# Kernel optimization log

Measured on AMD Instinct MI355X. Metric: run time of the kernel, lower is better.

## Reference

```python
import jax, jax.numpy as jnp
import numpy as np

UNITS = 1024
VOCAB = 50000
EMB = 512
SEQ = 256
BATCH = 256


def setup_inputs() -> dict:
    key = jax.random.key(0)
    ks = jax.random.split(key, 9)
    s = lambda fan_in: 1.0 / np.sqrt(fan_in)
    return {
        "sentences": jax.random.randint(ks[0], (BATCH, SEQ), 0, VOCAB),
        "emb_table": jax.random.normal(ks[1], (VOCAB, EMB), jnp.float32) * 0.05,
        # gate order: i, f, g(cell candidate), o
        "Wx": jax.random.normal(ks[2], (EMB, 4 * UNITS), jnp.float32) * s(EMB),
        "Wh": jax.random.normal(ks[3], (UNITS, 4 * UNITS), jnp.float32) * s(UNITS),
        "b": jnp.zeros((4 * UNITS,), jnp.float32),
        "W1": jax.random.normal(ks[4], (UNITS, 64), jnp.float32) * s(UNITS),
        "b1": jnp.zeros((64,), jnp.float32),
        "W2": jax.random.normal(ks[5], (64, 1), jnp.float32) * s(64),
        "b2": jnp.zeros((1,), jnp.float32),
    }


def _lstm_forward(emb_x, Wx, Wh, b):
    # emb_x: [B, T, E] -> final hidden state [B, U]
    B = emb_x.shape[0]
    U = Wh.shape[0]
    # precompute input projections for all timesteps: [T, B, 4U]
    x_proj = jnp.einsum('bte,eg->tbg', emb_x, Wx) + b

    def step(carry, xp):
        h, c = carry
        gates = xp + h @ Wh  # [B, 4U]
        i, f, g, o = jnp.split(gates, 4, axis=-1)
        i = jax.nn.sigmoid(i)
        f = jax.nn.sigmoid(f)
        g = jnp.tanh(g)
        o = jax.nn.sigmoid(o)
        c = f * c + i * g
        h = o * jnp.tanh(c)
        return (h, c), None

    h0 = jnp.zeros((B, U), emb_x.dtype)
    c0 = jnp.zeros((B, U), emb_x.dtype)
    (h, _), _ = jax.lax.scan(step, (h0, c0), x_proj)
    return h


def reference(sentences, emb_table, Wx, Wh, b, W1, b1, W2, b2):
    emb_x = emb_table[sentences]           # [B, T, E]
    h = _lstm_forward(emb_x, Wx, Wh, b)    # [B, U]
    hidden = h @ W1 + b1                   # Dense(64), linear activation
    logits = hidden @ W2 + b2              # Dense(1)
    return jax.nn.sigmoid(logits)          # [B, 1]
```

## Files before the change

kernel.cpp:

```cpp
#include <hip/hip_runtime.h>

#define B_ 256
#define T_ 256
#define E_ 512
#define U_ 1024
#define G_ 4096
#define V_ 50000
#define TC_ 32
#define NCH_ 8
#define NG_ 8
#define NS_ 32

typedef __bf16 bf16x8 __attribute__((ext_vector_type(8)));
typedef float f32x4 __attribute__((ext_vector_type(4)));
typedef unsigned short us8 __attribute__((ext_vector_type(8)));

__device__ __forceinline__ unsigned short f2bf(float f) {
  union { float f; unsigned u; } v; v.f = f;
  unsigned u = v.u;
  u = (u + 0x7FFFu + ((u >> 16) & 1u)) >> 16;
  return (unsigned short)u;
}
__device__ __forceinline__ float bf2f(unsigned short h) {
  union { unsigned u; float f; } v; v.u = ((unsigned)h) << 16;
  return v.f;
}
__device__ __forceinline__ float sigm_(float x) { return 1.f / (1.f + __expf(-x)); }
__device__ __forceinline__ float tanh_(float x) { return 2.f / (1.f + __expf(-2.f * x)) - 1.f; }

__device__ __forceinline__ void gload16(const void* g, void* l) {
  __builtin_amdgcn_global_load_lds((const __attribute__((address_space(1))) void*)g,
                                   (__attribute__((address_space(3))) void*)l, 16, 0, 0);
}
__device__ __forceinline__ void gload16c(const void* g, void* l) {
  __builtin_amdgcn_global_load_lds((const __attribute__((address_space(1))) void*)g,
                                   (__attribute__((address_space(3))) void*)l, 16, 0, 1);
}

__device__ __forceinline__ int orig_col3(int p) {
  return (((p >> 5) & 3) << 10) + ((p >> 7) << 5) + (p & 31);
}

__global__ void cvt_bf16_kernel(const float* __restrict__ in, unsigned short* __restrict__ out, long n) {
  long i = (((long)blockIdx.x * blockDim.x) + threadIdx.x) << 3;
  long stride = ((long)gridDim.x * blockDim.x) << 3;
  for (; i < n; i += stride) {
    float4 x = *(const float4*)(in + i);
    float4 y = *(const float4*)(in + i + 4);
    us8 v;
    v[0] = f2bf(x.x); v[1] = f2bf(x.y); v[2] = f2bf(x.z); v[3] = f2bf(x.w);
    v[4] = f2bf(y.x); v[5] = f2bf(y.y); v[6] = f2bf(y.z); v[7] = f2bf(y.w);
    *(us8*)(out + i) = v;
  }
}

__global__ void pack_wx_kernel(const float* __restrict__ w, unsigned short* __restrict__ out, int total) {
  int t = blockIdx.x * blockDim.x + threadIdx.x;
  if (t >= total) return;
  int kb = t >> 12, n = t & 4095;
  int oc = orig_col3(n);
  us8 v;
#pragma unroll
  for (int ki = 0; ki < 8; ki++) v[ki] = f2bf(w[(size_t)(kb * 8 + ki) * G_ + oc]);
  *(us8*)(out + (size_t)t * 8) = v;
}

__global__ void pack_wh4_kernel(const float* __restrict__ w, unsigned short* __restrict__ out) {
  int t = blockIdx.x * blockDim.x + threadIdx.x;
  int lane = t & 63;
  int nt  = (t >> 6) & 3;
  int ks  = (t >> 8) & 7;
  int ksl = (t >> 11) & 3;
  int nh  = (t >> 13) & 1;
  int s   = t >> 14;
  int k0 = ksl * 256 + ks * 32 + (lane >> 4) * 8;
  int oc = orig_col3(s * 128 + nh * 64 + nt * 16 + (lane & 15));
  us8 v;
#pragma unroll
  for (int i = 0; i < 8; i++) v[i] = f2bf(w[(size_t)(k0 + i) * G_ + oc]);
  *(us8*)(out + (size_t)t * 8) = v;
}

#define XP_BM 128
#define XP_BN 128
#define XP_KC 64
__global__ __launch_bounds__(256, 2) void xproj_kernel(
    const int* __restrict__ sent, const unsigned short* __restrict__ embb,
    const unsigned short* __restrict__ wxp, const float* __restrict__ bias,
    unsigned short* __restrict__ xp, int t0)
{
  __shared__ __align__(16) unsigned short sA[2][XP_BM * XP_KC];
  __shared__ __align__(16) unsigned short sB[2][XP_KC * XP_BN];
  __shared__ int tok[XP_BM];

  const int tid = threadIdx.x;
  const int lane = tid & 63;
  const int wid = tid >> 6;
  const int m0 = blockIdx.x * XP_BM;
  const int n0 = blockIdx.y * XP_BN;

  if (tid < XP_BM) {
    int row = m0 + tid;
    int tl = row >> 8, b = row & 255;
    tok[tid] = sent[b * T_ + t0 + tl];
  }
  __syncthreads();

  auto stageA = [&](int bf, int kc) {
#pragma unroll
    for (int ii = 0; ii < 4; ii++) {
      int i = wid * 4 + ii;
      int m = i * 8 + (lane >> 3);
      int cl = lane & 7;
      gload16(embb + (size_t)tok[m] * E_ + kc + ((cl ^ (m & 7)) << 3), &sA[bf][i * 512]);
    }
  };
  auto stageB = [&](int bf, int kc) {
    int kb0 = kc >> 3;
#pragma unroll
    for (int jj = 0; jj < 4; jj++) {
      int j = wid * 4 + jj;
      int r = j >> 1;
      int nl = ((j & 1) << 6) + lane;
      int n = nl ^ r;
      gload16(wxp + ((size_t)(kb0 + r) * G_ + n0 + n) * 8, &sB[bf][j * 512]);
    }
  };

  f32x4 acc[4][4];
#pragma unroll
  for (int i = 0; i < 4; i++)
#pragma unroll
    for (int j = 0; j < 4; j++) acc[i][j] = f32x4{0.f, 0.f, 0.f, 0.f};

  const int wm = wid >> 1, wn = wid & 1;

  stageA(0, 0); stageB(0, 0);
  for (int it = 0; it < E_ / XP_KC; it++) {
    int bf = it & 1;
    __syncthreads();
    if (it < E_ / XP_KC - 1) { stageA(bf ^ 1, (it + 1) * XP_KC); stageB(bf ^ 1, (it + 1) * XP_KC); }
#pragma unroll
    for (int kk = 0; kk < 2; kk++) {
      int c = (kk << 2) + (lane >> 4);
      bf16x8 a[4], b[4];
#pragma unroll
      for (int ms = 0; ms < 4; ms++) {
        int m = (wm << 6) + (ms << 4) + (lane & 15);
        a[ms] = *(const bf16x8*)&sA[bf][m * 64 + ((c ^ (m & 7)) << 3)];
      }
#pragma unroll
      for (int ns = 0; ns < 4; ns++) {
        int n = (wn << 6) + (ns << 4) + (lane & 15);
        b[ns] = *(const bf16x8*)&sB[bf][((c << 7) + (n ^ c)) << 3];
      }
#pragma unroll
      for (int ms = 0; ms < 4; ms++)
#pragma unroll
        for (int ns = 0; ns < 4; ns++)
          acc[ms][ns] = __builtin_amdgcn_mfma_f32_16x16x32_bf16(a[ms], b[ns], acc[ms][ns], 0, 0, 0);
    }
  }

#pragma unroll
  for (int ns = 0; ns < 4; ns++) {
    int col = n0 + (wn << 6) + (ns << 4) + (lane & 15);
    float bv = bias[orig_col3(col)];
#pragma unroll
    for (int ms = 0; ms < 4; ms++) {
      int rbase = m0 + (wm << 6) + (ms << 4) + ((lane >> 4) << 2);
#pragma unroll
      for (int rr = 0; rr < 4; rr++)
        xp[(size_t)(rbase + rr) * G_ + col] = f2bf(acc[ms][ns][rr] + bv);
    }
  }
}

__global__ __launch_bounds__(512, 2) void scan_kernel(
    const unsigned short* __restrict__ xpc,
    const unsigned short* __restrict__ whp4,
    unsigned short* __restrict__ hbuf,
    float* __restrict__ cst,
    int* __restrict__ flags,
    int t0)
{
  __shared__ __align__(16) unsigned short sA[32 * 1024];
  __shared__ float sEx[4][32][131];

  const int tid = threadIdx.x, lane = tid & 63, w = tid >> 6;
  const int ksl = w & 3, nh = w >> 2;
  const int g = (int)blockIdx.x & 7, s = (int)blockIdx.x >> 3;
  const int m0g = g * 32, u0 = s * 32;
  const int rx = lane & 7, hi = lane >> 4, lo = lane & 15;

  bf16x8 wh[8][4];
  {
    const bf16x8* wb = (const bf16x8*)whp4 + ((((size_t)s * 2 + nh) * 4 + ksl) * 32) * 64;
#pragma unroll
    for (int ks = 0; ks < 8; ks++)
#pragma unroll
      for (int nt = 0; nt < 4; nt++)
        wh[ks][nt] = wb[(ks * 4 + nt) * 64 + lane];
  }

  const int r_e = tid >> 4, ue = (tid & 15) * 2;
  const size_t ci = (size_t)(m0g + r_e) * U_ + u0 + ue;
  float c0v = cst[ci], c1v = cst[ci + 1];

  const char* abase0 = (const char*)sA + (size_t)lo * 2048;
  const char* abase1 = abase0 + 16 * 2048;

  for (int ts = 0; ts < TC_; ts++) {
    const int t = t0 + ts;

    const unsigned short* xb = xpc + ((size_t)ts * B_ + (m0g + r_e)) * G_ + s * 128;
    unsigned xiv = *(const unsigned*)(xb + ue);
    unsigned xfv = *(const unsigned*)(xb + 32 + ue);
    unsigned xgv = *(const unsigned*)(xb + 64 + ue);
    unsigned xov = *(const unsigned*)(xb + 96 + ue);

    if (t > 0) {
      const int* fp = flags + g * 32 + (lane & 31);
      int v;
      do { v = __hip_atomic_load(fp, __ATOMIC_RELAXED, __HIP_MEMORY_SCOPE_AGENT); }
      while (__any(v < t));
    }

    const unsigned short* hsrc = hbuf + (size_t)(t & 1) * (B_ * U_) + (size_t)m0g * U_;
#pragma unroll
    for (int jj = 0; jj < 8; jj++) {
      int j = w * 8 + jj;
      int r = j >> 1, k2 = j & 1;
      gload16c(hsrc + (size_t)r * U_ + (((k2 << 6) | (lane ^ (r & 7))) << 3),
               &sA[r * 1024 + k2 * 512]);
    }
    __syncthreads();

    f32x4 acc[2][4];
#pragma unroll
    for (int mt = 0; mt < 2; mt++)
#pragma unroll
      for (int nt = 0; nt < 4; nt++) acc[mt][nt] = f32x4{0.f, 0.f, 0.f, 0.f};
#pragma unroll
    for (int ks = 0; ks < 8; ks++) {
      int c = ksl * 32 + ks * 4 + hi;
      int off = (c ^ rx) << 4;
      bf16x8 a0 = *(const bf16x8*)(abase0 + off);
      bf16x8 a1 = *(const bf16x8*)(abase1 + off);
#pragma unroll
      for (int nt = 0; nt < 4; nt++) {
        acc[0][nt] = __builtin_amdgcn_mfma_f32_16x16x32_bf16(a0, wh[ks][nt], acc[0][nt], 0, 0, 0);
        acc[1][nt] = __builtin_amdgcn_mfma_f32_16x16x32_bf16(a1, wh[ks][nt], acc[1][nt], 0, 0, 0);
      }
    }

#pragma unroll
    for (int mt = 0; mt < 2; mt++)
#pragma unroll
      for (int nt = 0; nt < 4; nt++)
#pragma unroll
        for (int rr = 0; rr < 4; rr++)
          sEx[ksl][mt * 16 + hi * 4 + rr][nh * 64 + nt * 16 + lo] = acc[mt][nt][rr];
    __syncthreads();

    {
      float cn[2]; unsigned hv = 0;
#pragma unroll
      for (int j = 0; j < 2; j++) {
        int u = ue + j;
        float gi = sEx[0][r_e][u]      + sEx[1][r_e][u]      + sEx[2][r_e][u]      + sEx[3][r_e][u]      + bf2f((unsigned short)(j ? (xiv >> 16) : xiv));
        float gf = sEx[0][r_e][32 + u] + sEx[1][r_e][32 + u] + sEx[2][r_e][32 + u] + sEx[3][r_e][32 + u] + bf2f((unsigned short)(j ? (xfv >> 16) : xfv));
        float gg = sEx[0][r_e][64 + u] + sEx[1][r_e][64 + u] + sEx[2][r_e][64 + u] + sEx[3][r_e][64 + u] + bf2f((unsigned short)(j ? (xgv >> 16) : xgv));
        float go = sEx[0][r_e][96 + u] + sEx[1][r_e][96 + u] + sEx[2][r_e][96 + u] + sEx[3][r_e][96 + u] + bf2f((unsigned short)(j ? (xov >> 16) : xov));
        float co = j ? c1v : c0v;
        float cv = sigm_(gf) * co + sigm_(gi) * tanh_(gg);
        cn[j] = cv;
        hv |= (unsigned)f2bf(sigm_(go) * tanh_(cv)) << (16 * j);
      }
      c0v = cn[0]; c1v = cn[1];
      *(unsigned*)(hbuf + (size_t)((t + 1) & 1) * (B_ * U_) + ci) = hv;
    }
    __syncthreads();
    if (tid == 0)
      __hip_atomic_store(flags + g * 32 + s, t + 1, __ATOMIC_RELAXED, __HIP_MEMORY_SCOPE_AGENT);
  }

  cst[ci] = c0v; cst[ci + 1] = c1v;
}

__global__ __launch_bounds__(256) void dense_kernel(
    const unsigned short* __restrict__ h, const float* __restrict__ W1, const float* __restrict__ b1,
    const float* __restrict__ W2, const float* __restrict__ b2, float* __restrict__ out)
{
  int tid = threadIdx.x, j = tid & 63, kq = tid >> 6;
  const unsigned short* hr = h + (size_t)blockIdx.x * U_;
  float s = 0.f;
#pragma unroll 8
  for (int k = kq * 256; k < kq * 256 + 256; k++) s += bf2f(hr[k]) * W1[k * 64 + j];
  __shared__ float red[4][64];
  red[kq][j] = s;
  __syncthreads();
  if (tid < 64) {
    float hid = red[0][j] + red[1][j] + red[2][j] + red[3][j] + b1[j];
    float p = hid * W2[j];
#pragma unroll
    for (int off = 32; off; off >>= 1) p += __shfl_down(p, off, 64);
    if (j == 0) out[blockIdx.x] = 1.f / (1.f + __expf(-(p + b2[0])));
  }
}

extern "C" void kernel_launch(void* const* d_in, const int* in_sizes, int n_in,
                              void* d_out, int out_size, void* d_ws, size_t ws_size,
                              hipStream_t stream) {
  const int*   sent = (const int*)d_in[0];
  const float* emb  = (const float*)d_in[1];
  const float* Wx   = (const float*)d_in[2];
  const float* Wh   = (const float*)d_in[3];
  const float* bias = (const float*)d_in[4];
  const float* W1   = (const float*)d_in[5];
  const float* b1   = (const float*)d_in[6];
  const float* W2   = (const float*)d_in[7];
  const float* b2   = (const float*)d_in[8];
  float* out = (float*)d_out;

  char* ws = (char*)d_ws;
  size_t off = 0;
  auto alloc = [&](size_t bytes) { void* p = ws + off; off += (bytes + 255) & ~(size_t)255; return p; };
  unsigned short* embb = (unsigned short*)alloc((size_t)V_ * E_ * 2);
  unsigned short* wxp  = (unsigned short*)alloc((size_t)E_ * G_ * 2);
  unsigned short* whp4 = (unsigned short*)alloc((size_t)U_ * G_ * 2);
  unsigned short* xpc  = (unsigned short*)alloc((size_t)TC_ * B_ * G_ * 2);
  unsigned short* hbuf = (unsigned short*)alloc((size_t)2 * B_ * U_ * 2);
  float*          cst  = (float*)alloc((size_t)B_ * U_ * 4);
  int*            flg  = (int*)alloc((size_t)NG_ * 32 * 4);

  hipLaunchKernelGGL(cvt_bf16_kernel, dim3(12500), dim3(256), 0, stream, emb, embb, (long)V_ * E_);
  hipLaunchKernelGGL(pack_wx_kernel, dim3((E_ / 8) * G_ / 256), dim3(256), 0, stream, Wx, wxp, (E_ / 8) * G_);
  hipLaunchKernelGGL(pack_wh4_kernel, dim3(2048), dim3(256), 0, stream, Wh, whp4);
  hipMemsetAsync(hbuf, 0, (size_t)B_ * U_ * 2, stream);
  hipMemsetAsync(cst, 0, (size_t)B_ * U_ * 4, stream);
  hipMemsetAsync(flg, 0, (size_t)NG_ * 32 * 4, stream);

  for (int ch = 0; ch < NCH_; ch++) {
    hipLaunchKernelGGL(xproj_kernel, dim3(TC_ * B_ / XP_BM, G_ / XP_BN), dim3(256), 0, stream,
                       sent, embb, wxp, bias, xpc, ch * TC_);
    hipLaunchKernelGGL(scan_kernel, dim3(NG_ * NS_), dim3(512), 0, stream,
                       xpc, whp4, hbuf, cst, flg, ch * TC_);
  }
  hipLaunchKernelGGL(dense_kernel, dim3(B_), dim3(256), 0, stream,
                     hbuf , W1, b1, W2, b2, out);
}
```

Before: 1.561 ms.

## Replace per-block flag polling with per-step atomic counters and per-wave h loads

Each step's inter-block sync now uses a per-(timestep, group) atomic counter. A single lane polls it and releases the other waves through a shared-memory flag, replacing polling of 32 flags by every wave. Each wave now loads only its own K-slice of h into a private LDS region and waits on vmcnt, removing a block-wide __syncthreads before the MFMA loop. The spin loop has an iteration cap, and visibility of h written by other blocks relies on relaxed atomics, so there is some ordering risk.

```diff
diff --git a/kernel.cpp b/kernel.cpp
--- a/kernel.cpp
+++ b/kernel.cpp
@@ -181,17 +181,19 @@
     const unsigned short* __restrict__ whp4,
     unsigned short* __restrict__ hbuf,
     float* __restrict__ cst,
-    int* __restrict__ flags,
+    int* __restrict__ cnt,
     int t0)
 {
-  __shared__ __align__(16) unsigned short sA[32 * 1024];
+  __shared__ __align__(16) unsigned short sA[4][32][256];
   __shared__ float sEx[4][32][131];
+  __shared__ int sready;
 
   const int tid = threadIdx.x, lane = tid & 63, w = tid >> 6;
   const int ksl = w & 3, nh = w >> 2;
   const int g = (int)blockIdx.x & 7, s = (int)blockIdx.x >> 3;
   const int m0g = g * 32, u0 = s * 32;
-  const int rx = lane & 7, hi = lane >> 4, lo = lane & 15;
+  const int hi = lane >> 4, lo = lane & 15;
+  const int rx = lo & 7;
 
   bf16x8 wh[8][4];
   {
@@ -207,8 +209,11 @@
   const size_t ci = (size_t)(m0g + r_e) * U_ + u0 + ue;
   float c0v = cst[ci], c1v = cst[ci + 1];
 
-  const char* abase0 = (const char*)sA + (size_t)lo * 2048;
-  const char* abase1 = abase0 + 16 * 2048;
+  if (tid == 0) sready = t0 - 1;
+  __syncthreads();
+
+  const char* ab0 = (const char*)&sA[ksl][0][0] + (size_t)lo * 512;
+  const char* ab1 = ab0 + 16 * 512;
 
   for (int ts = 0; ts < TC_; ts++) {
     const int t = t0 + ts;
@@ -220,21 +225,28 @@
     unsigned xov = *(const unsigned*)(xb + 96 + ue);
 
     if (t > 0) {
-      const int* fp = flags + g * 32 + (lane & 31);
-      int v;
-      do { v = __hip_atomic_load(fp, __ATOMIC_RELAXED, __HIP_MEMORY_SCOPE_AGENT); }
-      while (__any(v < t));
-    }
-
-    const unsigned short* hsrc = hbuf + (size_t)(t & 1) * (B_ * U_) + (size_t)m0g * U_;
-#pragma unroll
-    for (int jj = 0; jj < 8; jj++) {
-      int j = w * 8 + jj;
-      int r = j >> 1, k2 = j & 1;
-      gload16c(hsrc + (size_t)r * U_ + (((k2 << 6) | (lane ^ (r & 7))) << 3),
-               &sA[r * 1024 + k2 * 512]);
-    }
-    __syncthreads();
+      if (w == 0) {
+        if (lane == 0) {
+          const int* cp = cnt + (size_t)(t * NG_ + g) * 32;
+          int v, it = 0;
+          do { v = __hip_atomic_load(cp, __ATOMIC_RELAXED, __HIP_MEMORY_SCOPE_AGENT); }
+          while (v < NS_ && ++it < (1 << 26));
+          __hip_atomic_store(&sready, t, __ATOMIC_RELAXED, __HIP_MEMORY_SCOPE_WORKGROUP);
+        }
+      } else {
+        while (__hip_atomic_load(&sready, __ATOMIC_RELAXED, __HIP_MEMORY_SCOPE_WORKGROUP) < t)
+          __builtin_amdgcn_s_sleep(1);
+      }
+    }
+
+    const unsigned short* hsrc = hbuf + (size_t)(t & 1) * (B_ * U_) + (size_t)m0g * U_ + ksl * 256;
+#pragma unroll
+    for (int j = 0; j < 16; j++) {
+      int row = 2 * j + (lane >> 5);
+      gload16c(hsrc + (size_t)row * U_ + (((lane & 31) ^ (row & 7)) << 3),
+               &sA[ksl][2 * j][0]);
+    }
+    asm volatile("s_waitcnt vmcnt(0)" ::: "memory");
 
     f32x4 acc[2][4];
 #pragma unroll
@@ -243,10 +255,9 @@
       for (int nt = 0; nt < 4; nt++) acc[mt][nt] = f32x4{0.f, 0.f, 0.f, 0.f};
 #pragma unroll
     for (int ks = 0; ks < 8; ks++) {
-      int c = ksl * 32 + ks * 4 + hi;
-      int off = (c ^ rx) << 4;
-      bf16x8 a0 = *(const bf16x8*)(abase0 + off);
-      bf16x8 a1 = *(const bf16x8*)(abase1 + off);
+      int off = (((ks * 4 + hi) ^ rx) << 4);
+      bf16x8 a0 = *(const bf16x8*)(ab0 + off);
+      bf16x8 a1 = *(const bf16x8*)(ab1 + off);
 #pragma unroll
       for (int nt = 0; nt < 4; nt++) {
         acc[0][nt] = __builtin_amdgcn_mfma_f32_16x16x32_bf16(a0, wh[ks][nt], acc[0][nt], 0, 0, 0);
@@ -282,7 +293,8 @@
     }
     __syncthreads();
     if (tid == 0)
-      __hip_atomic_store(flags + g * 32 + s, t + 1, __ATOMIC_RELAXED, __HIP_MEMORY_SCOPE_AGENT);
+      __hip_atomic_fetch_add(cnt + (size_t)((t + 1) * NG_ + g) * 32, 1,
+                             __ATOMIC_RELAXED, __HIP_MEMORY_SCOPE_AGENT);
   }
 
   cst[ci] = c0v; cst[ci + 1] = c1v;
@@ -332,20 +344,20 @@
   unsigned short* xpc  = (unsigned short*)alloc((size_t)TC_ * B_ * G_ * 2);
   unsigned short* hbuf = (unsigned short*)alloc((size_t)2 * B_ * U_ * 2);
   float*          cst  = (float*)alloc((size_t)B_ * U_ * 4);
-  int*            flg  = (int*)alloc((size_t)NG_ * 32 * 4);
+  int*            cnt  = (int*)alloc((size_t)(T_ + 1) * NG_ * 32 * 4);
 
   hipLaunchKernelGGL(cvt_bf16_kernel, dim3(12500), dim3(256), 0, stream, emb, embb, (long)V_ * E_);
   hipLaunchKernelGGL(pack_wx_kernel, dim3((E_ / 8) * G_ / 256), dim3(256), 0, stream, Wx, wxp, (E_ / 8) * G_);
   hipLaunchKernelGGL(pack_wh4_kernel, dim3(2048), dim3(256), 0, stream, Wh, whp4);
   hipMemsetAsync(hbuf, 0, (size_t)B_ * U_ * 2, stream);
   hipMemsetAsync(cst, 0, (size_t)B_ * U_ * 4, stream);
-  hipMemsetAsync(flg, 0, (size_t)NG_ * 32 * 4, stream);
+  hipMemsetAsync(cnt, 0, (size_t)(T_ + 1) * NG_ * 32 * 4, stream);
 
   for (int ch = 0; ch < NCH_; ch++) {
     hipLaunchKernelGGL(xproj_kernel, dim3(TC_ * B_ / XP_BM, G_ / XP_BN), dim3(256), 0, stream,
                        sent, embb, wxp, bias, xpc, ch * TC_);
     hipLaunchKernelGGL(scan_kernel, dim3(NG_ * NS_), dim3(512), 0, stream,
-                       xpc, whp4, hbuf, cst, flg, ch * TC_);
+                       xpc, whp4, hbuf, cst, cnt, ch * TC_);
   }
   hipLaunchKernelGGL(dense_kernel, dim3(B_), dim3(256), 0, stream,
                      hbuf , W1, b1, W2, b2, out);
```

Result: slower. 1.604 ms (+2.8%).
